# Kernel optimization log

Hardware: AMD Instinct MI355X
Metric: run time of the kernel (lower is better)

The kernel has to match this reference:

```python
import jax, jax.numpy as jnp
import numpy as np

ALPHA, GAMMA = 0.25, 2.0
ACCEPT, REJECT = 0.5, 0.4
CLF_W, REG_W = 1.0, 50.0
SL1_R = 9.0  # reg_smooth_l1_loss_scaling_factor
EPS = 1e-4


def _calc_iou(a, b):
    # a: [A,4] anchors in yxyx ; b: [M,4] gt boxes in xyxy (as in original code)
    ay1, ax1, ay2, ax2 = a[:, 0], a[:, 1], a[:, 2], a[:, 3]
    bx1, by1, bx2, by2 = b[:, 0], b[:, 1], b[:, 2], b[:, 3]
    iw = jnp.clip(jnp.minimum(ax2[:, None], bx2) - jnp.maximum(ax1[:, None], bx1), 0.0)
    ih = jnp.clip(jnp.minimum(ay2[:, None], by2) - jnp.maximum(ay1[:, None], by1), 0.0)
    inter = iw * ih  # [A, M]
    aarea = ((ax2 - ax1) * (ay2 - ay1))[:, None]
    barea = (bx2 - bx1) * (by2 - by1)
    union = jnp.clip(aarea + barea - inter, 1e-8)
    return inter / union


def _single_image(clf, reg, ann, anchors, a_cx, a_cy, a_w, a_h):
    # clf: [A,C], reg: [A,4], ann: [M,5] (x1,y1,x2,y2,label; label=-1 => pad)
    clf = jnp.clip(clf, EPS, 1.0 - EPS)
    labels = ann[:, 4]
    valid = labels != -1.0  # [M]
    boxes = ann[:, :4]
    iou = _calc_iou(anchors, boxes)               # [A, M]
    iou = jnp.where(valid[None, :], iou, -1.0)    # invalid GT never matches
    iou_max = iou.max(axis=-1)                    # [A]
    iou_arg = iou.argmax(axis=-1)                 # [A]
    matched = iou_max > ACCEPT
    unmatched = iou_max < REJECT
    num_matched = matched.sum()
    # classification targets: -1 (ignore) by default, 0 for unmatched, one-hot for matched
    gt_lbl = labels[iou_arg].astype(jnp.int32) - 1  # [A]
    one_hot = jax.nn.one_hot(gt_lbl, clf.shape[-1], dtype=clf.dtype)
    tgt = jnp.where(matched[:, None], one_hot,
                    jnp.where(unmatched[:, None], 0.0, -1.0))
    pos = ALPHA * (1.0 - clf) ** GAMMA * (-jnp.log(clf))
    neg = (1.0 - ALPHA) * clf ** GAMMA * (-jnp.log(1.0 - clf))
    clf_losses = jnp.where(tgt == 1.0, pos, neg)
    clf_losses = jnp.where(tgt == -1.0, 0.0, clf_losses)
    clf_loss = clf_losses.sum() / jnp.maximum(1, num_matched).astype(clf.dtype)
    gb = boxes[iou_arg]  # [A,4] xyxy
    gw_raw = gb[:, 2] - gb[:, 0]
    gh_raw = gb[:, 3] - gb[:, 1]
    gcx = gb[:, 0] + 0.5 * gw_raw
    gcy = gb[:, 1] + 0.5 * gh_raw
    gw = jnp.clip(gw_raw, 1.0)
    gh = jnp.clip(gh_raw, 1.0)
    reg_t = jnp.stack(((gcy - a_cy) / a_h,
                       (gcx - a_cx) / a_w,
                       jnp.log(gh / a_h),
                       jnp.log(gw / a_w)), axis=-1)  # [A,4] (dy,dx,dh,dw)
    d = jnp.abs(SL1_R * (reg - reg_t))
    sl1 = jnp.where(d < 1.0, 0.5 * d * d, d - 0.5)
    sl1 = jnp.where(matched[:, None], sl1, 0.0)
    denom = jnp.maximum(1, 4 * num_matched).astype(clf.dtype)
    reg_loss = jnp.where(num_matched > 0, sl1.sum() / denom, 0.0)
    return clf_loss, reg_loss


def setup_inputs() -> dict:
    key = jax.random.key(0)
    ks = jax.random.split(key, 12)
    B, A, C, M = 8, 49104, 90, 32
    clf = jax.random.uniform(ks[0], (B, A, C), jnp.float32)
    reg = jax.random.normal(ks[1], (B, A, 4), jnp.float32)
    # anchors in yxyx, all with positive width/height
    y1 = jax.random.uniform(ks[2], (A,)) * 480.0
    x1 = jax.random.uniform(ks[3], (A,)) * 480.0
    ah = jax.random.uniform(ks[4], (A,)) * 120.0 + 8.0
    aw = jax.random.uniform(ks[5], (A,)) * 120.0 + 8.0
    anchors = jnp.stack([y1, x1, y1 + ah, x1 + aw], axis=-1)[None].astype(jnp.float32)
    # annotations: xyxy boxes + label in [1, C]; ~half padded with label -1
    bx1 = jax.random.uniform(ks[6], (B, M)) * 400.0
    by1 = jax.random.uniform(ks[7], (B, M)) * 400.0
    bw = jax.random.uniform(ks[8], (B, M)) * 100.0 + 20.0
    bh = jax.random.uniform(ks[9], (B, M)) * 100.0 + 20.0
    lbl = jax.random.randint(ks[10], (B, M), 1, C + 1).astype(jnp.float32)
    lbl = jnp.where(jax.random.uniform(ks[11], (B, M)) < 0.6, lbl, -1.0)
    ann = jnp.stack([bx1, by1, bx1 + bw, by1 + bh, lbl], axis=-1).astype(jnp.float32)
    return {"classifications": clf, "regressions": reg, "anchors": anchors, "annotations": ann}


def reference(classifications, regressions, anchors, annotations):
    anc = anchors.squeeze()  # [A,4] yxyx
    a_w = anc[:, 3] - anc[:, 1]
    a_h = anc[:, 2] - anc[:, 0]
    a_cx = anc[:, 1] + 0.5 * a_w
    a_cy = anc[:, 0] + 0.5 * a_h
    clf = jnp.clip(classifications, EPS, 1.0 - EPS)
    clf_l, reg_l = jax.vmap(_single_image, in_axes=(0, 0, 0, None, None, None, None, None))(
        clf, regressions, annotations, anc, a_cx, a_cy, a_w, a_h)
    return CLF_W * clf_l.mean(), REG_W * reg_l.mean()
```

## Files before the change

kernel.cpp:

```cpp
#include <hip/hip_runtime.h>


namespace {
constexpr int B_N = 8;
constexpr int A_N = 49104;
constexpr int C_N = 90;
constexpr int M_N = 32;
constexpr float EPSF   = 1e-4f;
constexpr float ACCEPT = 0.5f;
constexpr float REJECT = 0.4f;
constexpr float SL1R   = 9.0f;
constexpr float CLFW   = 1.0f;
constexpr float REGW   = 50.0f;
constexpr float LN2    = 0.69314718055994530942f;

constexpr int APB = 256;
constexpr int NBX = (A_N + APB - 1) / APB;

__device__ __forceinline__ float clampx(float x) {
    return __builtin_amdgcn_fmed3f(x, EPSF, 1.0f - EPSF);
}
__device__ __forceinline__ float neg_term(float x) {
    x = clampx(x);
    return 0.75f * x * x * (-__logf(1.0f - x));
}
__device__ __forceinline__ float pos_term(float x) {
    x = clampx(x);
    float o = 1.0f - x;
    return 0.25f * o * o * (-__logf(x));
}
}

__global__ void fused_kernel(const float* __restrict__ anchors,
                             const float* __restrict__ reg,
                             const float* __restrict__ ann,
                             const float* __restrict__ clf,
                             float4* __restrict__ part)
{
    __shared__ float sann[M_N * 5];
    __shared__ int   s_match[APB];
    __shared__ int   s_ign[APB];
    __shared__ int   s_nm, s_ni;
    __shared__ float sred[4][4];

    const int b   = blockIdx.y;
    const int a0  = blockIdx.x * APB;
    const int tid = threadIdx.x;
    if (tid < M_N * 5) sann[tid] = ann[b * M_N * 5 + tid];
    if (tid == 0) { s_nm = 0; s_ni = 0; }
    __syncthreads();

    float cnt  = 0.0f;
    float rsum = 0.0f;
    float corr = 0.0f;
    const int i = a0 + tid;

    if (i < A_N) {
        const float4 av = ((const float4*)anchors)[i];
        const float ay1 = av.x, ax1 = av.y, ay2 = av.z, ax2 = av.w;
        const float aw = ax2 - ax1, ah = ay2 - ay1;
        const float aarea = aw * ah;

        float best = -3.4e38f;
        int   arg  = 0;
        #pragma unroll 8
        for (int j = 0; j < M_N; ++j) {
            const float bx1 = sann[j*5+0], by1 = sann[j*5+1];
            const float bx2 = sann[j*5+2], by2 = sann[j*5+3];
            const float lb  = sann[j*5+4];
            float iw = fminf(ax2, bx2) - fmaxf(ax1, bx1); iw = fmaxf(iw, 0.0f);
            float ih = fminf(ay2, by2) - fmaxf(ay1, by1); ih = fmaxf(ih, 0.0f);
            const float inter = iw * ih;
            const float barea = (bx2 - bx1) * (by2 - by1);
            const float uni   = fmaxf(aarea + barea - inter, 1e-8f);
            float iou = inter / uni;
            if (lb == -1.0f) iou = -1.0f;
            if (iou > best) { best = iou; arg = j; }
        }

        const bool matched   = best > ACCEPT;
        const bool unmatched = best < REJECT;

        if (matched) {
            const int s = (int)sann[arg*5+4] - 1;
            cnt = 1.0f;
            const int slot = atomicAdd(&s_nm, 1);
            s_match[slot] = (tid << 8) | s;
            const float bx1 = sann[arg*5+0], by1 = sann[arg*5+1];
            const float bx2 = sann[arg*5+2], by2 = sann[arg*5+3];
            const float gwr = bx2 - bx1, ghr = by2 - by1;
            const float gcx = bx1 + 0.5f * gwr, gcy = by1 + 0.5f * ghr;
            const float gw  = fmaxf(gwr, 1.0f), gh = fmaxf(ghr, 1.0f);
            const float acx = ax1 + 0.5f * aw, acy = ay1 + 0.5f * ah;
            const float t0 = (gcy - acy) / ah;
            const float t1 = (gcx - acx) / aw;
            const float t2 = __logf(gh / ah);
            const float t3 = __logf(gw / aw);
            const float4 rv = ((const float4*)reg)[b * A_N + i];
            float d;
            d = fabsf(SL1R * (rv.x - t0)); rsum += (d < 1.0f) ? 0.5f*d*d : d - 0.5f;
            d = fabsf(SL1R * (rv.y - t1)); rsum += (d < 1.0f) ? 0.5f*d*d : d - 0.5f;
            d = fabsf(SL1R * (rv.z - t2)); rsum += (d < 1.0f) ? 0.5f*d*d : d - 0.5f;
            d = fabsf(SL1R * (rv.w - t3)); rsum += (d < 1.0f) ? 0.5f*d*d : d - 0.5f;
        } else if (!unmatched) {
            const int slot = atomicAdd(&s_ni, 1);
            s_ign[slot] = tid;
        }
    }
    __syncthreads();

    const int nA  = min(APB, A_N - a0);
    const int nF4 = nA * C_N / 4;
    const float4* __restrict__ p =
        (const float4*)(clf + ((size_t)b * A_N + a0) * C_N);

    float S = 0.0f;

    auto w4 = [](float4 v) -> float {
        float s = 0.0f;
        const float x0 = clampx(v.x), x1 = clampx(v.y);
        const float x2 = clampx(v.z), x3 = clampx(v.w);
        s = fmaf(x0 * x0, __log2f(1.0f - x0), s);
        s = fmaf(x1 * x1, __log2f(1.0f - x1), s);
        s = fmaf(x2 * x2, __log2f(1.0f - x2), s);
        s = fmaf(x3 * x3, __log2f(1.0f - x3), s);
        return s;
    };

    int f = tid;
    #pragma unroll 1
    for (; f + 768 < nF4; f += 1024) {
        const float4 v0 = p[f];
        const float4 v1 = p[f + 256];
        const float4 v2 = p[f + 512];
        const float4 v3 = p[f + 768];
        S += w4(v0) + w4(v1) + w4(v2) + w4(v3);
    }
    for (; f < nF4; f += 256) S += w4(p[f]);

    const int nm = s_nm, ni = s_ni;
    for (int k = tid; k < nm; k += 256) {
        const int packed = s_match[k];
        const int a  = packed >> 8;
        const int sc = packed & 0xFF;
        const float x = clf[((size_t)b * A_N + a0 + a) * C_N + sc];
        corr += pos_term(x) - neg_term(x);
    }
    const int wid  = tid >> 6;
    const int lane = tid & 63;
    for (int e = wid; e < ni; e += 4) {
        const int a = s_ign[e];
        const float2* __restrict__ r2 =
            (const float2*)(clf + ((size_t)b * A_N + a0 + a) * C_N);
        if (lane < 45) {
            const float2 u = r2[lane];
            corr -= neg_term(u.x) + neg_term(u.y);
        }
    }

    #pragma unroll
    for (int off = 32; off > 0; off >>= 1) {
        cnt  += __shfl_down(cnt,  off);
        rsum += __shfl_down(rsum, off);
        S    += __shfl_down(S,    off);
        corr += __shfl_down(corr, off);
    }
    if (lane == 0) {
        sred[wid][0] = cnt; sred[wid][1] = rsum;
        sred[wid][2] = S;   sred[wid][3] = corr;
    }
    __syncthreads();
    if (tid == 0) {
        float c = 0.f, r = 0.f, ss = 0.f, k = 0.f;
        #pragma unroll
        for (int w = 0; w < 4; ++w) {
            c += sred[w][0]; r += sred[w][1]; ss += sred[w][2]; k += sred[w][3];
        }
        part[b * NBX + blockIdx.x] = make_float4(c, r, ss, k);
    }
}

__global__ void finalize_kernel(const float4* __restrict__ part,
                                float*        __restrict__ out)
{
    __shared__ float s_cnt[B_N], s_rsum[B_N], s_S[B_N], s_corr[B_N];
    const int tid = threadIdx.x;
    const int b   = tid >> 5;
    const int j   = tid & 31;

    float cnt = 0.f, rsum = 0.f, S = 0.f, corr = 0.f;
    #pragma unroll
    for (int k = 0; k < NBX / 32; ++k) {
        const float4 m = part[b * NBX + j + 32 * k];
        cnt += m.x; rsum += m.y; S += m.z; corr += m.w;
    }
    #pragma unroll
    for (int off = 16; off > 0; off >>= 1) {
        cnt  += __shfl_down(cnt,  off, 32);
        rsum += __shfl_down(rsum, off, 32);
        S    += __shfl_down(S,    off, 32);
        corr += __shfl_down(corr, off, 32);
    }
    if (j == 0) { s_cnt[b] = cnt; s_rsum[b] = rsum; s_S[b] = S; s_corr[b] = corr; }
    __syncthreads();
    if (tid == 0) {
        float cl = 0.0f, rl = 0.0f;
        #pragma unroll
        for (int bb = 0; bb < B_N; ++bb) {
            const float n = s_cnt[bb];
            const float clf_total = -0.75f * LN2 * s_S[bb] + s_corr[bb];
            cl += clf_total / fmaxf(1.0f, n);
            if (n > 0.0f) rl += s_rsum[bb] / (4.0f * n);
        }
        out[0] = CLFW * (cl / (float)B_N);
        out[1] = REGW * (rl / (float)B_N);
    }
}

extern "C" void kernel_launch(void* const* d_in, const int* in_sizes, int n_in,
                              void* d_out, int out_size, void* d_ws, size_t ws_size,
                              hipStream_t stream) {
    const float* clf     = (const float*)d_in[0];
    const float* reg     = (const float*)d_in[1];
    const float* anchors = (const float*)d_in[2];
    const float* ann     = (const float*)d_in[3];
    float*  out  = (float*)d_out;
    float4* part = (float4*)d_ws;

    {
        dim3 grid(NBX, B_N);
        fused_kernel<<<grid, 256, 0, stream>>>(anchors, reg, ann, clf, part);
    }
    finalize_kernel<<<1, 256, 0, stream>>>(part, out);
}
```

Measured before the change: 215.1 us.

## Split dense classification stream into its own kernel separate from IoU matching

Moves the dense sum over all classification probabilities out of the per-anchor matching kernel into a dedicated grid-stride streaming kernel with fixed 256 blocks per image. The matching kernel now only does IoU, regression and sparse corrections, and the finalize kernel combines both partial buffers. The intent is a cleaner bandwidth-bound stream with better occupancy, decoupled from the matching work. The cost is an extra launch and a second pass that rereads classification rows for matched and ignored anchors, which the fused version may have found in cache.

```diff
diff --git a/kernel.cpp b/kernel.cpp
--- a/kernel.cpp
+++ b/kernel.cpp
@@ -14,8 +14,10 @@
 constexpr float REGW   = 50.0f;
 constexpr float LN2    = 0.69314718055994530942f;
 
-constexpr int APB = 256;
-constexpr int NBX = (A_N + APB - 1) / APB;
+constexpr int APB  = 256;
+constexpr int NBX  = (A_N + APB - 1) / APB;
+constexpr int SBLK = 256;
+constexpr int NF4  = A_N * C_N / 4;
 
 __device__ __forceinline__ float clampx(float x) {
     return __builtin_amdgcn_fmed3f(x, EPSF, 1.0f - EPSF);
@@ -29,19 +31,62 @@
     float o = 1.0f - x;
     return 0.25f * o * o * (-__logf(x));
 }
-}
-
-__global__ void fused_kernel(const float* __restrict__ anchors,
+__device__ __forceinline__ float w4(float4 v) {
+    float s = 0.0f;
+    const float x0 = clampx(v.x), x1 = clampx(v.y);
+    const float x2 = clampx(v.z), x3 = clampx(v.w);
+    s = fmaf(x0 * x0, __log2f(1.0f - x0), s);
+    s = fmaf(x1 * x1, __log2f(1.0f - x1), s);
+    s = fmaf(x2 * x2, __log2f(1.0f - x2), s);
+    s = fmaf(x3 * x3, __log2f(1.0f - x3), s);
+    return s;
+}
+}
+
+__global__ __launch_bounds__(256, 8)
+void clf_stream_kernel(const float* __restrict__ clf,
+                       float*       __restrict__ partS)
+{
+    const int b   = blockIdx.y;
+    const int tid = threadIdx.x;
+    const float4* __restrict__ p =
+        (const float4*)(clf + (size_t)b * A_N * C_N);
+
+    constexpr int STRIDE = SBLK * 256;
+    float S = 0.0f;
+    int f = blockIdx.x * 256 + tid;
+
+    #pragma unroll 1
+    for (; f + 3 * STRIDE < NF4; f += 4 * STRIDE) {
+        const float4 v0 = p[f];
+        const float4 v1 = p[f +     STRIDE];
+        const float4 v2 = p[f + 2 * STRIDE];
+        const float4 v3 = p[f + 3 * STRIDE];
+        S += w4(v0) + w4(v1) + w4(v2) + w4(v3);
+    }
+    for (; f < NF4; f += STRIDE) S += w4(p[f]);
+
+    __shared__ float sred[4];
+    #pragma unroll
+    for (int off = 32; off > 0; off >>= 1) S += __shfl_down(S, off);
+    const int wid = tid >> 6, lane = tid & 63;
+    if (lane == 0) sred[wid] = S;
+    __syncthreads();
+    if (tid == 0)
+        partS[b * SBLK + blockIdx.x] = sred[0] + sred[1] + sred[2] + sred[3];
+}
+
+__global__ void match_kernel(const float* __restrict__ anchors,
                              const float* __restrict__ reg,
                              const float* __restrict__ ann,
                              const float* __restrict__ clf,
-                             float4* __restrict__ part)
+                             float4* __restrict__ partM)
 {
     __shared__ float sann[M_N * 5];
     __shared__ int   s_match[APB];
     __shared__ int   s_ign[APB];
     __shared__ int   s_nm, s_ni;
-    __shared__ float sred[4][4];
+    __shared__ float sred[4][3];
 
     const int b   = blockIdx.y;
     const int a0  = blockIdx.x * APB;
@@ -109,35 +154,6 @@
     }
     __syncthreads();
 
-    const int nA  = min(APB, A_N - a0);
-    const int nF4 = nA * C_N / 4;
-    const float4* __restrict__ p =
-        (const float4*)(clf + ((size_t)b * A_N + a0) * C_N);
-
-    float S = 0.0f;
-
-    auto w4 = [](float4 v) -> float {
-        float s = 0.0f;
-        const float x0 = clampx(v.x), x1 = clampx(v.y);
-        const float x2 = clampx(v.z), x3 = clampx(v.w);
-        s = fmaf(x0 * x0, __log2f(1.0f - x0), s);
-        s = fmaf(x1 * x1, __log2f(1.0f - x1), s);
-        s = fmaf(x2 * x2, __log2f(1.0f - x2), s);
-        s = fmaf(x3 * x3, __log2f(1.0f - x3), s);
-        return s;
-    };
-
-    int f = tid;
-    #pragma unroll 1
-    for (; f + 768 < nF4; f += 1024) {
-        const float4 v0 = p[f];
-        const float4 v1 = p[f + 256];
-        const float4 v2 = p[f + 512];
-        const float4 v3 = p[f + 768];
-        S += w4(v0) + w4(v1) + w4(v2) + w4(v3);
-    }
-    for (; f < nF4; f += 256) S += w4(p[f]);
-
     const int nm = s_nm, ni = s_ni;
     for (int k = tid; k < nm; k += 256) {
         const int packed = s_match[k];
@@ -162,25 +178,24 @@
     for (int off = 32; off > 0; off >>= 1) {
         cnt  += __shfl_down(cnt,  off);
         rsum += __shfl_down(rsum, off);
-        S    += __shfl_down(S,    off);
         corr += __shfl_down(corr, off);
     }
     if (lane == 0) {
-        sred[wid][0] = cnt; sred[wid][1] = rsum;
-        sred[wid][2] = S;   sred[wid][3] = corr;
+        sred[wid][0] = cnt; sred[wid][1] = rsum; sred[wid][2] = corr;
     }
     __syncthreads();
     if (tid == 0) {
-        float c = 0.f, r = 0.f, ss = 0.f, k = 0.f;
+        float c = 0.f, r = 0.f, k = 0.f;
         #pragma unroll
         for (int w = 0; w < 4; ++w) {
-            c += sred[w][0]; r += sred[w][1]; ss += sred[w][2]; k += sred[w][3];
-        }
-        part[b * NBX + blockIdx.x] = make_float4(c, r, ss, k);
-    }
-}
-
-__global__ void finalize_kernel(const float4* __restrict__ part,
+            c += sred[w][0]; r += sred[w][1]; k += sred[w][2];
+        }
+        partM[b * NBX + blockIdx.x] = make_float4(c, r, k, 0.0f);
+    }
+}
+
+__global__ void finalize_kernel(const float4* __restrict__ partM,
+                                const float*  __restrict__ partS,
                                 float*        __restrict__ out)
 {
     __shared__ float s_cnt[B_N], s_rsum[B_N], s_S[B_N], s_corr[B_N];
@@ -191,9 +206,13 @@
     float cnt = 0.f, rsum = 0.f, S = 0.f, corr = 0.f;
     #pragma unroll
     for (int k = 0; k < NBX / 32; ++k) {
-        const float4 m = part[b * NBX + j + 32 * k];
-        cnt += m.x; rsum += m.y; S += m.z; corr += m.w;
-    }
+        const float4 m = partM[b * NBX + j + 32 * k];
+        cnt += m.x; rsum += m.y; corr += m.z;
+    }
+    #pragma unroll
+    for (int k = 0; k < SBLK / 32; ++k)
+        S += partS[b * SBLK + j + 32 * k];
+
     #pragma unroll
     for (int off = 16; off > 0; off >>= 1) {
         cnt  += __shfl_down(cnt,  off, 32);
@@ -224,12 +243,18 @@
     const float* reg     = (const float*)d_in[1];
     const float* anchors = (const float*)d_in[2];
     const float* ann     = (const float*)d_in[3];
-    float*  out  = (float*)d_out;
-    float4* part = (float4*)d_ws;
-
+    float* out = (float*)d_out;
+
+    float4* partM = (float4*)d_ws;
+    float*  partS = (float*)((char*)d_ws + B_N * NBX * sizeof(float4));
+
+    {
+        dim3 grid(SBLK, B_N);
+        clf_stream_kernel<<<grid, 256, 0, stream>>>(clf, partS);
+    }
     {
         dim3 grid(NBX, B_N);
-        fused_kernel<<<grid, 256, 0, stream>>>(anchors, reg, ann, clf, part);
-    }
-    finalize_kernel<<<1, 256, 0, stream>>>(part, out);
-}
+        match_kernel<<<grid, 256, 0, stream>>>(anchors, reg, ann, clf, partM);
+    }
+    finalize_kernel<<<1, 256, 0, stream>>>(partM, partS, out);
+}
```

Result: slower. 226.6 us (+5.4%).
